# Kernel tuning notes

Measured on AMD Instinct MI355X. Metric: run time of the kernel, lower is better.

The kernel has to match this reference:

```python
import jax, jax.numpy as jnp
import numpy as np

N_GRAPHS = 64
NEG_SLOPE = 0.2


def gat_conv(x, src, dst, n_nodes, W, a_src, a_dst, b):
    # PyG GATConv (heads=1): h = x @ W; e_ij = LeakyReLU(a_src.h_j + a_dst.h_i)
    # softmax over incoming edges of each destination node, then weighted sum.
    h = x @ W                                  # [N, F_out]
    alpha_s = h @ a_src                        # [N]
    alpha_d = h @ a_dst                        # [N]
    e = jax.nn.leaky_relu(alpha_s[src] + alpha_d[dst], NEG_SLOPE)  # [E]
    m = jax.ops.segment_max(e, dst, num_segments=n_nodes)          # stable softmax
    ex = jnp.exp(e - m[dst])
    denom = jax.ops.segment_sum(ex, dst, num_segments=n_nodes)
    alpha = ex / (denom[dst] + 1e-16)                              # [E]
    out = jax.ops.segment_sum(h[src] * alpha[:, None], dst, num_segments=n_nodes)
    return out + b


def setup_inputs() -> dict:
    key = jax.random.key(0)
    ks = jax.random.split(key, 16)
    N, E, D, H = 50000, 1600000, 128, 64
    x = jax.random.normal(ks[0], (N, D), dtype=jnp.float32)
    edge_index = jax.random.randint(ks[1], (2, E), 0, N, dtype=jnp.int64)
    batch = jnp.sort(jax.random.randint(ks[2], (N,), 0, N_GRAPHS, dtype=jnp.int64))
    def glorot(k, shape):
        lim = float(np.sqrt(6.0 / (shape[0] + shape[-1])))
        return jax.random.uniform(k, shape, jnp.float32, -lim, lim)
    return {
        "x": x, "edge_index": edge_index, "batch": batch,
        "W1": glorot(ks[3], (D, H)),
        "a_src1": glorot(ks[4], (H,)), "a_dst1": glorot(ks[5], (H,)),
        "b1": jnp.zeros((H,), jnp.float32),
        "W2": glorot(ks[6], (H, 2 * H)),
        "a_src2": glorot(ks[7], (2 * H,)), "a_dst2": glorot(ks[8], (2 * H,)),
        "b2": jnp.zeros((2 * H,), jnp.float32),
        "Wfc": glorot(ks[9], (2 * H, H)),
        "bfc": jnp.zeros((H,), jnp.float32),
    }


def reference(x, edge_index, batch, W1, a_src1, a_dst1, b1, W2, a_src2, a_dst2, b2, Wfc, bfc):
    n = x.shape[0]
    # PyG GATConv default add_self_loops=True
    loops = jnp.arange(n, dtype=edge_index.dtype)
    src = jnp.concatenate([edge_index[0], loops])
    dst = jnp.concatenate([edge_index[1], loops])
    h = jax.nn.relu(gat_conv(x, src, dst, n, W1, a_src1, a_dst1, b1))
    h = jax.nn.relu(gat_conv(h, src, dst, n, W2, a_src2, a_dst2, b2))
    # global_mean_pool over batch vector
    sums = jax.ops.segment_sum(h, batch, num_segments=N_GRAPHS)
    cnts = jax.ops.segment_sum(jnp.ones((n,), h.dtype), batch, num_segments=N_GRAPHS)
    pooled = sums / jnp.maximum(cnts, 1.0)[:, None]
    # dropout is identity in eval mode
    return pooled @ Wfc + bfc
```

## Files before the change

kernel.cpp:

```cpp
#include <hip/hip_runtime.h>
#include <hip/hip_fp16.h>

#define WAVE 64

constexpr int D_IN = 128;
constexpr int F1 = 64;
constexpr int F2 = 128;
constexpr int NG = 64;
constexpr float NEG = 0.2f;
constexpr int NBLK1 = 512;

using f16x8 = __attribute__((ext_vector_type(8))) _Float16;
using f32x4 = __attribute__((ext_vector_type(4))) float;

__device__ __forceinline__ float lrelu(float x){ return x > 0.f ? x : NEG * x; }

__global__ void k_hist(const int* __restrict__ src, const int* __restrict__ dst,
                       int E, int N, int NB, int chunk, int* __restrict__ cnt1,
                       int* __restrict__ done){
  __shared__ int hist[256];
  int b = blockIdx.x;
  if (b == 0 && threadIdx.x == 0) *done = 0;
  for (int t = threadIdx.x; t < NB; t += blockDim.x) hist[t] = 0;
  __syncthreads();
  int Et = E + N;
  int s0 = b * chunk, s1 = min(s0 + chunk, Et);
  for (int i = s0 + (int)threadIdx.x; i < s1; i += (int)blockDim.x){
    int d = (i < E) ? dst[i] : (i - E);
    atomicAdd(&hist[d >> 8], 1);
  }
  __syncthreads();
  for (int t = threadIdx.x; t < NB; t += blockDim.x) cnt1[t * NBLK1 + b] = hist[t];
}

__global__ void k_colscan(int* __restrict__ cnt1, int* __restrict__ btot,
                          int* __restrict__ done, int NB, int Et,
                          int* __restrict__ bbase, int* __restrict__ off, int N,
                          float* __restrict__ pool, int* __restrict__ cnt){
  __shared__ int lds[256];
  __shared__ int isLast;
  int b = blockIdx.x;
  int t = threadIdx.x;
  int v0 = cnt1[b * NBLK1 + 2 * t], v1 = cnt1[b * NBLK1 + 2 * t + 1];
  int p = v0 + v1;
  lds[t] = p; __syncthreads();
  #pragma unroll
  for (int s = 1; s < 256; s <<= 1){
    int u = (t >= s) ? lds[t - s] : 0;
    __syncthreads(); lds[t] += u; __syncthreads();
  }
  int epre = lds[t] - p;
  cnt1[b * NBLK1 + 2 * t] = epre;
  cnt1[b * NBLK1 + 2 * t + 1] = epre + v0;
  if (t == 255) btot[b] = lds[255];

  __threadfence();
  if (t == 0) isLast = (atomicAdd(done, 1) == (int)gridDim.x - 1);
  __syncthreads();
  if (!isLast) return;
  __threadfence();

  int v = (t < NB) ? btot[t] : 0;
  lds[t] = v; __syncthreads();
  #pragma unroll
  for (int s = 1; s < 256; s <<= 1){
    int u = (t >= s) ? lds[t - s] : 0;
    __syncthreads(); lds[t] += u; __syncthreads();
  }
  if (t < NB) bbase[t] = lds[t] - v;
  if (t == 0){ bbase[NB] = Et; off[N] = Et; }
  for (int i = t; i < NG * F2; i += 256) pool[i] = 0.f;
  if (t < NG) cnt[t] = 0;
}

__global__ void k_scatter1(const int* __restrict__ src, const int* __restrict__ dst,
                           int E, int N, int NB, int chunk,
                           const int* __restrict__ cnt1, const int* __restrict__ bbase,
                           int* __restrict__ tmp){
  __shared__ int cur[256];
  int b = blockIdx.x;
  for (int t = threadIdx.x; t < NB; t += blockDim.x) cur[t] = bbase[t] + cnt1[t * NBLK1 + b];
  __syncthreads();
  int Et = E + N;
  int s0 = b * chunk, s1 = min(s0 + chunk, Et);
  for (int i = s0 + (int)threadIdx.x; i < s1; i += (int)blockDim.x){
    int s, d;
    if (i < E){ s = src[i]; d = dst[i]; } else { s = d = i - E; }
    int bk = d >> 8;
    int p = atomicAdd(&cur[bk], 1);
    tmp[p] = (s << 8) | (d & 255);
  }
}

__global__ void k_sort2(const int* __restrict__ tmp, const int* __restrict__ bbase,
                        int N, int* __restrict__ off, int* __restrict__ csr_src){
  __shared__ int hist[256];
  __shared__ int pre[256];
  int b = blockIdx.x;
  int t = threadIdx.x;
  hist[t] = 0;
  __syncthreads();
  int g0 = bbase[b], g1 = bbase[b + 1];
  for (int i = g0 + t; i < g1; i += 256) atomicAdd(&hist[tmp[i] & 255], 1);
  __syncthreads();
  int v = hist[t];
  pre[t] = v; __syncthreads();
  #pragma unroll
  for (int s = 1; s < 256; s <<= 1){
    int u = (t >= s) ? pre[t - s] : 0;
    __syncthreads(); pre[t] += u; __syncthreads();
  }
  int ex = pre[t] - v;
  int node = (b << 8) + t;
  if (node < N) off[node] = g0 + ex;
  hist[t] = ex;
  __syncthreads();
  for (int i = g0 + t; i < g1; i += 256){
    int e = tmp[i];
    int p = g0 + atomicAdd(&hist[e & 255], 1);
    csr_src[p] = e >> 8;
  }
}

template<int FI, int FO, bool AF32>
__global__ void k_gemm_mfma(const void* __restrict__ Av, const float* __restrict__ W,
                            const float* __restrict__ avs, const float* __restrict__ avd,
                            __half* __restrict__ Ch, float* __restrict__ as_, float* __restrict__ ad_,
                            int M){
  constexpr int NT = FO / 16;
  constexpr int KT = FI / 32;
  constexpr int MT = 2;
  __shared__ _Float16 blds[NT * KT * 64 * 8];

  int tid = threadIdx.x;
  for (int fl = tid; fl < NT * KT * 64; fl += 256){
    int l = fl & 63, kt = (fl >> 6) % KT, nt = fl / (64 * KT);
    int n = nt * 16 + (l & 15), kb = kt * 32 + (l >> 4) * 8;
    f16x8 v;
    #pragma unroll
    for (int i = 0; i < 8; ++i) v[i] = (_Float16)W[(size_t)(kb + i) * FO + n];
    *(f16x8*)&blds[(size_t)fl * 8] = v;
  }
  __syncthreads();

  int lane = tid & 63, wave = tid >> 6;
  int rbase = lane & 15, kgrp = lane >> 4;
  int r0 = blockIdx.x * (MT * 16 * 4) + wave * (MT * 16);

  f32x4 c[MT][NT];
  #pragma unroll
  for (int mt = 0; mt < MT; ++mt)
    #pragma unroll
    for (int nt = 0; nt < NT; ++nt)
      c[mt][nt] = (f32x4){0.f, 0.f, 0.f, 0.f};

  for (int kt = 0; kt < KT; ++kt){
    f16x8 a[MT];
    #pragma unroll
    for (int mt = 0; mt < MT; ++mt){
      int arow = min(r0 + mt * 16 + rbase, M - 1);
      if (AF32){
        const float* ap = (const float*)Av + (size_t)arow * FI + kt * 32 + kgrp * 8;
        float4 p0 = *(const float4*)ap;
        float4 p1 = *(const float4*)(ap + 4);
        a[mt][0] = (_Float16)p0.x; a[mt][1] = (_Float16)p0.y;
        a[mt][2] = (_Float16)p0.z; a[mt][3] = (_Float16)p0.w;
        a[mt][4] = (_Float16)p1.x; a[mt][5] = (_Float16)p1.y;
        a[mt][6] = (_Float16)p1.z; a[mt][7] = (_Float16)p1.w;
      } else {
        const __half* ap = (const __half*)Av + (size_t)arow * FI + kt * 32 + kgrp * 8;
        a[mt] = *(const f16x8*)ap;
      }
    }
    #pragma unroll
    for (int nt = 0; nt < NT; ++nt){
      f16x8 b = *(f16x8*)&blds[(size_t)((nt * KT + kt) * 64 + lane) * 8];
      #pragma unroll
      for (int mt = 0; mt < MT; ++mt)
        c[mt][nt] = __builtin_amdgcn_mfma_f32_16x16x32_f16(a[mt], b, c[mt][nt], 0, 0, 0);
    }
  }

  float avs_v[NT], avd_v[NT];
  #pragma unroll
  for (int nt = 0; nt < NT; ++nt){
    avs_v[nt] = avs[nt * 16 + rbase];
    avd_v[nt] = avd[nt * 16 + rbase];
  }
  #pragma unroll
  for (int mt = 0; mt < MT; ++mt){
    #pragma unroll
    for (int i = 0; i < 4; ++i){
      int grow = r0 + mt * 16 + kgrp * 4 + i;
      bool ok = grow < M;
      float s1 = 0.f, s2 = 0.f;
      #pragma unroll
      for (int nt = 0; nt < NT; ++nt){
        float d = c[mt][nt][i];
        if (ok) Ch[(size_t)grow * FO + nt * 16 + rbase] = __float2half(d);
        s1 += d * avs_v[nt];
        s2 += d * avd_v[nt];
      }
      #pragma unroll
      for (int msk = 1; msk <= 8; msk <<= 1){
        s1 += __shfl_xor(s1, msk);
        s2 += __shfl_xor(s2, msk);
      }
      if (ok && rbase == 0){ as_[grow] = s1; ad_[grow] = s2; }
    }
  }
}

template<int F, int U>
__global__ void k_node(const int* __restrict__ off, const int* __restrict__ csr_src,
                       const float* __restrict__ as_, const float* __restrict__ ad_,
                       const __half* __restrict__ h, const float* __restrict__ bias,
                       __half* __restrict__ outh, int N){
  constexpr int LPR = F / 8;
  constexpr int EPW = 64 / LPR;
  int lane = threadIdx.x & (WAVE - 1);
  int wid = (int)((blockIdx.x * blockDim.x + threadIdx.x) >> 6);
  int node = __builtin_amdgcn_readfirstlane(wid);
  if (node >= N) return;
  int o0 = off[node], o1 = off[node + 1];
  float add = ad_[node];
  int q = lane / LPR;
  int cbase = (lane % LPR) * 8;

  float acc[8];
  #pragma unroll
  for (int i = 0; i < 8; ++i) acc[i] = 0.f;
  float wsum = 0.f;

  for (int jj = o0; jj < o1; jj += U * EPW){
    int s[U]; bool okv[U];
    #pragma unroll
    for (int u = 0; u < U; ++u){
      int j = jj + u * EPW + q;
      okv[u] = j < o1;
      s[u] = csr_src[okv[u] ? j : o0];
    }
    float araw[U];
    #pragma unroll
    for (int u = 0; u < U; ++u) araw[u] = as_[s[u]];
    f16x8 hv[U];
    #pragma unroll
    for (int u = 0; u < U; ++u) hv[u] = *(const f16x8*)(h + (size_t)s[u] * F + cbase);
    #pragma unroll
    for (int u = 0; u < U; ++u){
      float w = okv[u] ? __expf(lrelu(araw[u] + add)) : 0.f;
      wsum += w;
      #pragma unroll
      for (int i = 0; i < 8; ++i) acc[i] += w * (float)hv[u][i];
    }
  }

  #pragma unroll
  for (int m = LPR; m < 64; m <<= 1){
    #pragma unroll
    for (int i = 0; i < 8; ++i) acc[i] += __shfl_xor(acc[i], m);
    wsum += __shfl_xor(wsum, m);
  }

  if (q == 0){
    float inv = 1.f / (wsum + 1e-16f);
    f16x8 o;
    #pragma unroll
    for (int i = 0; i < 8; ++i){
      float v = fmaxf(acc[i] * inv + bias[cbase + i], 0.f);
      o[i] = (_Float16)v;
    }
    *(f16x8*)(outh + (size_t)node * F + cbase) = o;
  }
}

__global__ void k_pool(const __half* __restrict__ h, const int* __restrict__ batch,
                       float* __restrict__ pool, int* __restrict__ cnt, int N, int strip){
  int f = threadIdx.x;
  int n0 = blockIdx.x * strip;
  if (n0 >= N) return;
  int n1 = min(n0 + strip, N);
  int g = batch[n0];
  float acc = 0.f;
  int c = 0;
  for (int n = n0; n < n1; ++n){
    int gn = batch[n];
    if (gn != g){
      atomicAdd(&pool[g * F2 + f], acc);
      if (f == 0) atomicAdd(&cnt[g], c);
      acc = 0.f; c = 0; g = gn;
    }
    acc += __half2float(h[(size_t)n * F2 + f]);
    c++;
  }
  atomicAdd(&pool[g * F2 + f], acc);
  if (f == 0) atomicAdd(&cnt[g], c);
}

__global__ void k_fc(const float* __restrict__ pool, const int* __restrict__ cnt,
                     const float* __restrict__ Wfc, const float* __restrict__ bfc,
                     float* __restrict__ out){
  int g = blockIdx.x, o = threadIdx.x;
  __shared__ float p[F2];
  float invc = 1.f / fmaxf((float)cnt[g], 1.f);
  for (int k = threadIdx.x; k < F2; k += 64) p[k] = pool[g * F2 + k] * invc;
  __syncthreads();
  float acc = bfc[o];
  for (int k = 0; k < F2; ++k) acc += p[k] * Wfc[k * 64 + o];
  out[g * 64 + o] = acc;
}

extern "C" void kernel_launch(void* const* d_in, const int* in_sizes, int n_in,
                              void* d_out, int out_size, void* d_ws, size_t ws_size,
                              hipStream_t stream){
  const float* x    = (const float*)d_in[0];
  const int*   edge = (const int*)d_in[1];
  const int*   batch= (const int*)d_in[2];
  const float* W1   = (const float*)d_in[3];
  const float* av_s1= (const float*)d_in[4];
  const float* av_d1= (const float*)d_in[5];
  const float* b1   = (const float*)d_in[6];
  const float* W2   = (const float*)d_in[7];
  const float* av_s2= (const float*)d_in[8];
  const float* av_d2= (const float*)d_in[9];
  const float* b2   = (const float*)d_in[10];
  const float* Wfc  = (const float*)d_in[11];
  const float* bfc  = (const float*)d_in[12];
  float* out = (float*)d_out;

  const int N  = in_sizes[2];
  const int E  = in_sizes[1] / 2;
  const int Et = E + N;
  const int NB = (N + 255) >> 8;
  const int* src = edge;
  const int* dst = edge + E;

  char* p = (char*)d_ws;
  auto alloc = [&](size_t bytes)->void*{
    void* r = (void*)p;
    p += (bytes + 255) & ~(size_t)255;
    return r;
  };
  __half* h1  = (__half*)alloc((size_t)N * F1 * 2);
  __half* h1r = (__half*)alloc((size_t)N * F1 * 2);
  __half* h2  = (__half*)alloc((size_t)N * F2 * 2);
  __half* h2r = (__half*)alloc((size_t)N * F2 * 2);
  float* as1  = (float*)alloc((size_t)N * 4);
  float* ad1  = (float*)alloc((size_t)N * 4);
  float* as2  = (float*)alloc((size_t)N * 4);
  float* ad2  = (float*)alloc((size_t)N * 4);
  float* pool = (float*)alloc((size_t)NG * F2 * 4);
  int* off    = (int*)alloc((size_t)(N + 1) * 4);
  int* csr_src= (int*)alloc((size_t)Et * 4);
  int* tmp    = (int*)alloc((size_t)Et * 4);
  int* cnt1   = (int*)alloc((size_t)256 * NBLK1 * 4);
  int* btot   = (int*)alloc((size_t)256 * 4);
  int* bbase  = (int*)alloc((size_t)257 * 4);
  int* cnt    = (int*)alloc((size_t)NG * 4);
  int* done   = (int*)alloc((size_t)256 * 4);

  int chunk = (Et + NBLK1 - 1) / NBLK1;
  k_hist<<<NBLK1, 256, 0, stream>>>(src, dst, E, N, NB, chunk, cnt1, done);
  k_colscan<<<NB, 256, 0, stream>>>(cnt1, btot, done, NB, Et, bbase, off, N, pool, cnt);
  k_scatter1<<<NBLK1, 256, 0, stream>>>(src, dst, E, N, NB, chunk, cnt1, bbase, tmp);
  k_sort2<<<NB, 256, 0, stream>>>(tmp, bbase, N, off, csr_src);

  int gemm_blocks = (N + 127) / 128;
  int node_blocks = (N + 3) / 4;

  k_gemm_mfma<D_IN, F1, true><<<gemm_blocks, 256, 0, stream>>>(x, W1, av_s1, av_d1,
                                                               h1, as1, ad1, N);
  k_node<F1, 4><<<node_blocks, 256, 0, stream>>>(off, csr_src, as1, ad1, h1, b1, h1r, N);

  k_gemm_mfma<F1, F2, false><<<gemm_blocks, 256, 0, stream>>>(h1r, W2, av_s2, av_d2,
                                                              h2, as2, ad2, N);
  k_node<F2, 6><<<node_blocks, 256, 0, stream>>>(off, csr_src, as2, ad2, h2, b2, h2r, N);

  int strip = 128;
  int pool_blocks = (N + strip - 1) / strip;
  k_pool<<<pool_blocks, F2, 0, stream>>>(h2r, batch, pool, cnt, N, strip);
  k_fc<<<NG, 64, 0, stream>>>(pool, cnt, Wfc, bfc, out);
}
```

Before: 207.0 us.

## Slice node features into eight column slabs so aggregation gathers stay cache-resident

Stores the GEMM outputs and the aggregated node features in a feature-sliced layout: eight separate N×(F/8) slabs instead of one row-major array. The GEMM A-loads, the pooling kernel and the aggregation kernel are all rewritten to index this layout. The aggregation kernel now launches eight times as many blocks, and each block gathers only one slab, so the randomly accessed working set per slice is small enough to stay in L2. The cost is that CSR index loads, source-score loads and exp weight computations are repeated for every slice, and each gather shrinks to a 16- or 32-byte fragment of a cache line.

Result: slower. 519.2 us (+150.9%).

```diff
diff --git a/kernel.cpp b/kernel.cpp
--- a/kernel.cpp
+++ b/kernel.cpp
@@ -130,6 +130,7 @@
   constexpr int NT = FO / 16;
   constexpr int KT = FI / 32;
   constexpr int MT = 2;
+  constexpr int CPS = FO / 8;
   __shared__ _Float16 blds[NT * KT * 64 * 8];
 
   int tid = threadIdx.x;
@@ -159,8 +160,9 @@
     #pragma unroll
     for (int mt = 0; mt < MT; ++mt){
       int arow = min(r0 + mt * 16 + rbase, M - 1);
+      int kb = kt * 32 + kgrp * 8;
       if (AF32){
-        const float* ap = (const float*)Av + (size_t)arow * FI + kt * 32 + kgrp * 8;
+        const float* ap = (const float*)Av + (size_t)arow * FI + kb;
         float4 p0 = *(const float4*)ap;
         float4 p1 = *(const float4*)(ap + 4);
         a[mt][0] = (_Float16)p0.x; a[mt][1] = (_Float16)p0.y;
@@ -168,7 +170,7 @@
         a[mt][4] = (_Float16)p1.x; a[mt][5] = (_Float16)p1.y;
         a[mt][6] = (_Float16)p1.z; a[mt][7] = (_Float16)p1.w;
       } else {
-        const __half* ap = (const __half*)Av + (size_t)arow * FI + kt * 32 + kgrp * 8;
+        const __half* ap = (const __half*)Av + ((size_t)(kb >> 3) * M + arow) * 8;
         a[mt] = *(const f16x8*)ap;
       }
     }
@@ -197,7 +199,10 @@
       #pragma unroll
       for (int nt = 0; nt < NT; ++nt){
         float d = c[mt][nt][i];
-        if (ok) Ch[(size_t)grow * FO + nt * 16 + rbase] = __float2half(d);
+        if (ok){
+          int col = nt * 16 + rbase;
+          Ch[((size_t)(col / CPS) * M + grow) * CPS + (col % CPS)] = __float2half(d);
+        }
         s1 += d * avs_v[nt];
         s2 += d * avd_v[nt];
       }
@@ -212,20 +217,24 @@
 }
 
 template<int F, int U>
-__global__ void k_node(const int* __restrict__ off, const int* __restrict__ csr_src,
-                       const float* __restrict__ as_, const float* __restrict__ ad_,
-                       const __half* __restrict__ h, const float* __restrict__ bias,
-                       __half* __restrict__ outh, int N){
-  constexpr int LPR = F / 8;
+__global__ void k_node_s(const int* __restrict__ off, const int* __restrict__ csr_src,
+                         const float* __restrict__ as_, const float* __restrict__ ad_,
+                         const __half* __restrict__ hs, const float* __restrict__ bias,
+                         __half* __restrict__ outs, int N){
+  constexpr int CPS = F / 8;
+  constexpr int LPR = CPS / 8;
   constexpr int EPW = 64 / LPR;
   int lane = threadIdx.x & (WAVE - 1);
-  int wid = (int)((blockIdx.x * blockDim.x + threadIdx.x) >> 6);
+  int bid = blockIdx.x;
+  int slice = bid & 7;
+  int wid = (bid >> 3) * 4 + (int)(threadIdx.x >> 6);
   int node = __builtin_amdgcn_readfirstlane(wid);
   if (node >= N) return;
   int o0 = off[node], o1 = off[node + 1];
   float add = ad_[node];
   int q = lane / LPR;
   int cbase = (lane % LPR) * 8;
+  const __half* hb = hs + (size_t)slice * N * CPS + cbase;
 
   float acc[8];
   #pragma unroll
@@ -245,7 +254,7 @@
     for (int u = 0; u < U; ++u) araw[u] = as_[s[u]];
     f16x8 hv[U];
     #pragma unroll
-    for (int u = 0; u < U; ++u) hv[u] = *(const f16x8*)(h + (size_t)s[u] * F + cbase);
+    for (int u = 0; u < U; ++u) hv[u] = *(const f16x8*)(hb + (size_t)s[u] * CPS);
     #pragma unroll
     for (int u = 0; u < U; ++u){
       float w = okv[u] ? __expf(lrelu(araw[u] + add)) : 0.f;
@@ -267,19 +276,20 @@
     f16x8 o;
     #pragma unroll
     for (int i = 0; i < 8; ++i){
-      float v = fmaxf(acc[i] * inv + bias[cbase + i], 0.f);
+      float v = fmaxf(acc[i] * inv + bias[slice * CPS + cbase + i], 0.f);
       o[i] = (_Float16)v;
     }
-    *(f16x8*)(outh + (size_t)node * F + cbase) = o;
-  }
-}
-
-__global__ void k_pool(const __half* __restrict__ h, const int* __restrict__ batch,
+    *(f16x8*)(outs + ((size_t)slice * N + node) * CPS + cbase) = o;
+  }
+}
+
+__global__ void k_pool(const __half* __restrict__ hs, const int* __restrict__ batch,
                        float* __restrict__ pool, int* __restrict__ cnt, int N, int strip){
   int f = threadIdx.x;
   int n0 = blockIdx.x * strip;
   if (n0 >= N) return;
   int n1 = min(n0 + strip, N);
+  const __half* hb = hs + (size_t)(f >> 4) * N * 16 + (f & 15);
   int g = batch[n0];
   float acc = 0.f;
   int c = 0;
@@ -290,7 +300,7 @@
       if (f == 0) atomicAdd(&cnt[g], c);
       acc = 0.f; c = 0; g = gn;
     }
-    acc += __half2float(h[(size_t)n * F2 + f]);
+    acc += __half2float(hb[(size_t)n * 16]);
     c++;
   }
   atomicAdd(&pool[g * F2 + f], acc);
@@ -366,15 +376,15 @@
   k_sort2<<<NB, 256, 0, stream>>>(tmp, bbase, N, off, csr_src);
 
   int gemm_blocks = (N + 127) / 128;
-  int node_blocks = (N + 3) / 4;
+  int node_blocks = ((N + 3) / 4) * 8;
 
   k_gemm_mfma<D_IN, F1, true><<<gemm_blocks, 256, 0, stream>>>(x, W1, av_s1, av_d1,
                                                                h1, as1, ad1, N);
-  k_node<F1, 4><<<node_blocks, 256, 0, stream>>>(off, csr_src, as1, ad1, h1, b1, h1r, N);
+  k_node_s<F1, 1><<<node_blocks, 256, 0, stream>>>(off, csr_src, as1, ad1, h1, b1, h1r, N);
 
   k_gemm_mfma<F1, F2, false><<<gemm_blocks, 256, 0, stream>>>(h1r, W2, av_s2, av_d2,
                                                               h2, as2, ad2, N);
-  k_node<F2, 6><<<node_blocks, 256, 0, stream>>>(off, csr_src, as2, ad2, h2, b2, h2r, N);
+  k_node_s<F2, 2><<<node_blocks, 256, 0, stream>>>(off, csr_src, as2, ad2, h2, b2, h2r, N);
 
   int strip = 128;
   int pool_blocks = (N + strip - 1) / strip;
```
